# Optimization experiments

Hardware: AMD Instinct MI355X
Metric: run time of the kernel (lower is better)

Reference implementation:

```python
import math
import jax, jax.numpy as jnp
import numpy as np

B, H, T, N, D = 2, 4, 2048, 2048, 256
THETA = 2.0 ** 16


def setup_inputs() -> dict:
    key = jax.random.key(0)
    kq, kv = jax.random.split(key)
    Q = jax.random.normal(kq, (B, H, T, N), dtype=jnp.float32)
    V = jax.random.normal(kv, (B, 1, T, D), dtype=jnp.float32)
    return {"Q": Q, "V": V}


def _rope(Q):
    """BDH RoPE: freqs quantized in pairs, phases wrapped mod 1 then scaled to radians."""
    b, h, t, n = Q.shape
    # quantize(arange(n), 2) -> [0,0,2,2,4,4,...]
    idx = (jnp.arange(n) // 2 * 2).astype(jnp.float32)
    freqs = 1.0 / (THETA ** (idx / n)) / (2.0 * math.pi)            # (N,)
    pos = jnp.arange(t, dtype=jnp.float32)[:, None]                  # (T,1)
    phases = (pos * freqs) % 1.0 * (2.0 * math.pi)                   # (T,N)
    cos, sin = jnp.cos(phases), jnp.sin(phases)
    # rotate pairs: even slot <- -odd, odd slot <- even
    q2 = Q.reshape(b, h, t, n // 2, 2)
    Qrot = jnp.stack((-q2[..., 1], q2[..., 0]), axis=-1).reshape(b, h, t, n)
    return Q * cos + Qrot * sin


def reference(Q, V):
    QR = _rope(Q)                                                    # (B,H,T,N)
    scores = jnp.einsum('bhtn,bhsn->bhts', QR, QR)                   # (B,H,T,T), no softmax
    # strict lower-triangular causal mask (diagonal excluded), as in .tril(diagonal=-1)
    mask = jnp.tril(jnp.ones((scores.shape[-2], scores.shape[-1]), dtype=scores.dtype), k=-1)
    scores = scores * mask
    return jnp.matmul(scores, V)                                     # (B,H,T,D) via broadcast over H
```

## Files before the change

### kernel.cpp

```cpp
#include <hip/hip_runtime.h>
#include <stdint.h>

#define Tn 2048
#define Nn 2048
#define Dn 256
#define NHEAD 8
#define NKI 16

typedef __attribute__((ext_vector_type(8))) short short8;
typedef __attribute__((ext_vector_type(4))) float f32x4;
typedef __attribute__((ext_vector_type(4))) int i32x4;

__device__ __forceinline__ uint16_t f2bf(float x) {
  uint32_t u = __float_as_uint(x);
  return (uint16_t)((u + 0x7FFFu + ((u >> 16) & 1u)) >> 16);
}

__device__ __forceinline__ void gload_lds16(const void* g, void* l) {
  __builtin_amdgcn_global_load_lds((const __attribute__((address_space(1))) uint32_t*)g,
                                   (__attribute__((address_space(3))) uint32_t*)l,
                                   16, 0, 0);
}

__global__ __launch_bounds__(256) void rope_kernel(const float* __restrict__ Q,
                                                   uint8_t* __restrict__ QR,
                                                   float* __restrict__ Sc,
                                                   const float* __restrict__ V,
                                                   uint16_t* __restrict__ VT) {
  const int tid = threadIdx.x;
  const int bx = blockIdx.x;
  {
    int o = bx * 256 + tid;
    int vt = o & (Tn - 1);
    int vd = (o >> 11) & (Dn - 1);
    int vb = o >> 19;
    VT[o] = f2bf(V[((size_t)vb * Tn + vt) * Dn + vd]);
  }
  const int wv = tid >> 6, L = tid & 63;
  const int row = bx * 4 + wv;
  const int t = row & (Tn - 1);
  const float* src = Q + (size_t)row * Nn;

  float o[32];
  float am = 1e-8f;
#pragma unroll
  for (int k = 0; k < 8; ++k) {
    const float4 q = *(const float4*)(src + L * 4 + 256 * k);
    int p0 = 2 * L + 128 * k;
    float f0 = exp2f(-(float)p0 * (1.0f / 64.0f)) * 0.15915494309189535f;
    float f1 = exp2f(-(float)(p0 + 1) * (1.0f / 64.0f)) * 0.15915494309189535f;
    float x0 = (float)t * f0, x1 = (float)t * f1;
    float r0 = x0 - floorf(x0), r1 = x1 - floorf(x1);
    float s0 = __builtin_amdgcn_sinf(r0), c0 = __builtin_amdgcn_cosf(r0);
    float s1 = __builtin_amdgcn_sinf(r1), c1 = __builtin_amdgcn_cosf(r1);
    float o0 = q.x * c0 - q.y * s0;
    float o1 = q.y * c0 + q.x * s0;
    float o2 = q.z * c1 - q.w * s1;
    float o3 = q.w * c1 + q.z * s1;
    o[4 * k] = o0; o[4 * k + 1] = o1; o[4 * k + 2] = o2; o[4 * k + 3] = o3;
    am = fmaxf(am, fmaxf(fmaxf(fabsf(o0), fabsf(o1)), fmaxf(fabsf(o2), fabsf(o3))));
  }
#pragma unroll
  for (int off = 32; off > 0; off >>= 1) am = fmaxf(am, __shfl_xor(am, off));
  const float sc = 127.0f / am;
#pragma unroll
  for (int k = 0; k < 8; ++k) {
    int q0 = min(127, max(-127, (int)rintf(o[4 * k] * sc)));
    int q1 = min(127, max(-127, (int)rintf(o[4 * k + 1] * sc)));
    int q2 = min(127, max(-127, (int)rintf(o[4 * k + 2] * sc)));
    int q3 = min(127, max(-127, (int)rintf(o[4 * k + 3] * sc)));
    uint32_t pk = (uint32_t)(q0 & 255) | ((uint32_t)(q1 & 255) << 8) |
                  ((uint32_t)(q2 & 255) << 16) | ((uint32_t)q3 << 24);
    *(uint32_t*)(QR + (size_t)row * Nn + L * 4 + 256 * k) = pk;
  }
  if (L == 0) Sc[row] = am * (1.0f / 127.0f);
}

__global__ __launch_bounds__(256, 4) void qkt_kernel(const uint8_t* __restrict__ QR,
                                                     const float* __restrict__ Sc,
                                                     uint16_t* __restrict__ S) {
  __shared__ __align__(16) char lds0[32768];
  const int bx = blockIdx.x;
  const int g = bx & 7;
  int p = bx >> 3;
  int ti, tj; bool diag;
  if (p < 120) {
    ti = 1; while (p >= ti) { p -= ti; ++ti; }
    tj = p; diag = false;
  } else {
    ti = p - 120; tj = ti; diag = true;
  }

  const int tid = threadIdx.x;
  const int wv = tid >> 6, l = tid & 63, l15 = l & 15, lg = l >> 4;
  const int wi = wv >> 1;
  const int wj = wv & 1;
  const bool active = !(diag && wi == 0 && wj == 1);
  const bool needmask = diag && (wi == wj);

  const uint8_t* QRh = QR + (size_t)g * Tn * Nn;
  const int r0 = tid >> 3;
  const int scg = (tid & 7) ^ (r0 & 7);
  const uint8_t* gI = QRh + (size_t)(ti * 128 + r0) * Nn + scg * 16;
  const uint8_t* gJ = QRh + (size_t)(tj * 128 + r0) * Nn + scg * 16;

  char* bufI = lds0;
  char* bufJ = lds0 + 16384;

  i32x4 acc[4][4];
#pragma unroll
  for (int mi = 0; mi < 4; ++mi)
#pragma unroll
    for (int nj = 0; nj < 4; ++nj) acc[mi][nj] = (i32x4){0, 0, 0, 0};

  for (int k0 = 0; k0 < NKI; ++k0) {
    const int ke = k0 * 128;
    __syncthreads();
#pragma unroll
    for (int rnd = 0; rnd < 4; ++rnd) {
      gload_lds16(gI + (size_t)rnd * 32 * Nn + ke, bufI + rnd * 4096 + wv * 1024);
      if (!diag) gload_lds16(gJ + (size_t)rnd * 32 * Nn + ke, bufJ + rnd * 4096 + wv * 1024);
    }
    __syncthreads();
    if (active) {
      const char* bI = bufI;
      const char* bJ = diag ? bufI : bufJ;
#pragma unroll
      for (int ks = 0; ks < 2; ++ks) {
        i32x4 ifr[4], jfr[4];
#pragma unroll
        for (int mi = 0; mi < 4; ++mi) {
          int row = wi * 64 + mi * 16 + l15;
          int c = (ks * 4 + lg) ^ (row & 7);
          ifr[mi] = *(const i32x4*)(bI + row * 128 + c * 16);
        }
#pragma unroll
        for (int nj = 0; nj < 4; ++nj) {
          int row = wj * 64 + nj * 16 + l15;
          int c = (ks * 4 + lg) ^ (row & 7);
          jfr[nj] = *(const i32x4*)(bJ + row * 128 + c * 16);
        }
        __builtin_amdgcn_s_setprio(1);
#pragma unroll
        for (int mi = 0; mi < 4; ++mi)
#pragma unroll
          for (int nj = 0; nj < 4; ++nj)
            acc[mi][nj] = __builtin_amdgcn_mfma_i32_16x16x64_i8(jfr[nj], ifr[mi], acc[mi][nj], 0, 0, 0);
        __builtin_amdgcn_s_setprio(0);
      }
    }
  }

  uint16_t* Sh = S + (size_t)g * Tn * Tn;
  const float* ScI = Sc + g * Tn + ti * 128;
  const float* ScJ = Sc + g * Tn + tj * 128;
  if (active) {
#pragma unroll
    for (int mi = 0; mi < 4; ++mi) {
      int iloc = wi * 64 + mi * 16 + l15;
      float si = ScI[iloc];
#pragma unroll
      for (int nj = 0; nj < 4; ++nj) {
        int jloc = wj * 64 + nj * 16 + lg * 4;
        float4 sj = *(const float4*)(ScJ + jloc);
        i32x4 a = acc[mi][nj];
        float v0 = (float)a[0] * si * sj.x;
        float v1 = (float)a[1] * si * sj.y;
        float v2 = (float)a[2] * si * sj.z;
        float v3 = (float)a[3] * si * sj.w;
        if (needmask) {
          if (jloc + 0 >= iloc) v0 = 0.f;
          if (jloc + 1 >= iloc) v1 = 0.f;
          if (jloc + 2 >= iloc) v2 = 0.f;
          if (jloc + 3 >= iloc) v3 = 0.f;
        }
        uint32_t lo = (uint32_t)f2bf(v0) | ((uint32_t)f2bf(v1) << 16);
        uint32_t hi = (uint32_t)f2bf(v2) | ((uint32_t)f2bf(v3) << 16);
        *(uint2*)(Sh + (size_t)(ti * 128 + iloc) * Tn + tj * 128 + jloc) = make_uint2(lo, hi);
      }
    }
  } else {
#pragma unroll
    for (int mi = 0; mi < 4; ++mi)
#pragma unroll
      for (int nj = 0; nj < 4; ++nj) {
        int iloc = wi * 64 + mi * 16 + l15;
        int jloc = wj * 64 + nj * 16 + lg * 4;
        *(uint2*)(Sh + (size_t)(ti * 128 + iloc) * Tn + tj * 128 + jloc) = make_uint2(0u, 0u);
      }
  }
}

__global__ __launch_bounds__(512) void pv_kernel(const uint16_t* __restrict__ S,
                                                 const uint16_t* __restrict__ VT,
                                                 float* __restrict__ O) {
  extern __shared__ char lds[];
  const int bx = blockIdx.x;
  const int g = bx & 7;
  const int b = g >> 2;
  const int jid = bx >> 3;
  const int dh = jid & 1;
  const int ti = 31 - (jid >> 1);
  const int nsteps = ti + 1;

  const int tid = threadIdx.x;
  const int w = tid >> 6, l = tid & 63, l15 = l & 15, lg = l >> 4;
  const int ih = w >> 2;
  const int dq = w & 3;

  const uint16_t* Sh = S + (size_t)g * Tn * Tn;
  const uint16_t* VTb = VT + (size_t)b * Dn * Tn;
  const int r0 = tid >> 3;
  const int scg = (tid & 7) ^ (r0 & 7);
  const uint16_t* gS = Sh + (size_t)(ti * 64 + r0) * Tn + scg * 8;
  const uint16_t* gV = VTb + (size_t)(dh * 128 + r0) * Tn + scg * 8;

  f32x4 acc[2][2];
#pragma unroll
  for (int ma = 0; ma < 2; ++ma)
#pragma unroll
    for (int ni = 0; ni < 2; ++ni) acc[ma][ni] = (f32x4){0.f, 0.f, 0.f, 0.f};

  auto stage = [&](int ke, int bsel) {
    char* bufS = lds + bsel * 24576;
    char* bufV = bufS + 8192;
    gload_lds16(gS + ke, bufS + w * 1024);
    gload_lds16(gV + ke, bufV + w * 1024);
    gload_lds16(gV + (size_t)64 * Tn + ke, bufV + 8192 + w * 1024);
  };

  stage(0, 0);
  if (nsteps > 1) stage(64, 1);

  int cur = 0;
  for (int jt = 0; jt < nsteps; ++jt) {
    if (jt + 1 < nsteps) { asm volatile("s_waitcnt vmcnt(3)" ::: "memory"); }
    else                 { asm volatile("s_waitcnt vmcnt(0)" ::: "memory"); }
    __builtin_amdgcn_s_barrier();
    if (jt + 2 < nsteps) {
      int nb = cur + 2; if (nb >= 3) nb -= 3;
      stage((jt + 2) * 64, nb);
    }
    const char* bS = lds + cur * 24576;
    const char* bV = bS + 8192;
#pragma unroll
    for (int ks = 0; ks < 2; ++ks) {
      short8 av[2], bs[2];
#pragma unroll
      for (int ma = 0; ma < 2; ++ma) {
        int row = dq * 32 + ma * 16 + l15;
        int c = (ks * 4 + lg) ^ (row & 7);
        av[ma] = *(const short8*)(bV + row * 128 + c * 16);
      }
#pragma unroll
      for (int ni = 0; ni < 2; ++ni) {
        int row = ih * 32 + ni * 16 + l15;
        int c = (ks * 4 + lg) ^ (row & 7);
        bs[ni] = *(const short8*)(bS + row * 128 + c * 16);
      }
      __builtin_amdgcn_s_setprio(1);
#pragma unroll
      for (int ma = 0; ma < 2; ++ma)
#pragma unroll
        for (int ni = 0; ni < 2; ++ni)
          acc[ma][ni] = __builtin_amdgcn_mfma_f32_16x16x32_bf16(av[ma], bs[ni], acc[ma][ni], 0, 0, 0);
      __builtin_amdgcn_s_setprio(0);
    }
    ++cur; if (cur >= 3) cur = 0;
  }

  float* Oh = O + (size_t)g * Tn * Dn;
#pragma unroll
  for (int ma = 0; ma < 2; ++ma)
#pragma unroll
    for (int ni = 0; ni < 2; ++ni) {
      int iloc = ih * 32 + ni * 16 + l15;
      int d0 = dh * 128 + dq * 32 + ma * 16 + lg * 4;
      *(f32x4*)(Oh + (size_t)(ti * 64 + iloc) * Dn + d0) = acc[ma][ni];
    }
}

extern "C" void kernel_launch(void* const* d_in, const int* in_sizes, int n_in,
                              void* d_out, int out_size, void* d_ws, size_t ws_size,
                              hipStream_t stream) {
  const float* Q = (const float*)d_in[0];
  const float* V = (const float*)d_in[1];
  float* O = (float*)d_out;

  uint8_t* QRw = (uint8_t*)d_ws;
  float*   ScW = (float*)(QRw + (size_t)NHEAD * Tn * Nn);
  uint16_t* VTw = (uint16_t*)(ScW + (size_t)NHEAD * Tn);
  uint16_t* Sw  = VTw + (size_t)2 * Dn * Tn;

  hipFuncSetAttribute((const void*)pv_kernel, hipFuncAttributeMaxDynamicSharedMemorySize, 73728);

  rope_kernel<<<4096, 256, 0, stream>>>(Q, QRw, ScW, V, VTw);
  qkt_kernel<<<1088, 256, 0, stream>>>(QRw, ScW, Sw);
  pv_kernel<<<512, 512, 73728, stream>>>(Sw, VTw, O);
}
```

Measured before the change: 95.20 us.

## Use 128x64 QK^T tiles with finer triangular enumeration and higher occupancy

The QK^T kernel moves from 128x128 tiles, where diagonal tiles are handled specially, to 128x64 tiles. These are enumerated over the lower triangle at 64-column granularity, giving 272 tiles per head instead of 136. Masking now uses global indices, and launch bounds rise to 5 blocks per CU with less LDS per block. The intent is to cut wasted work above the diagonal and improve load balance and occupancy. The cost is lower arithmetic intensity per tile and more blocks that each reload the I rows.

```diff
diff --git a/kernel.cpp b/kernel.cpp
--- a/kernel.cpp
+++ b/kernel.cpp
@@ -6,6 +6,7 @@
 #define Dn 256
 #define NHEAD 8
 #define NKI 16
+#define JPH 272
 
 typedef __attribute__((ext_vector_type(8))) short short8;
 typedef __attribute__((ext_vector_type(4))) float f32x4;
@@ -76,75 +77,72 @@
   if (L == 0) Sc[row] = am * (1.0f / 127.0f);
 }
 
-__global__ __launch_bounds__(256, 4) void qkt_kernel(const uint8_t* __restrict__ QR,
+__global__ __launch_bounds__(256, 5) void qkt_kernel(const uint8_t* __restrict__ QR,
                                                      const float* __restrict__ Sc,
                                                      uint16_t* __restrict__ S) {
-  __shared__ __align__(16) char lds0[32768];
+  __shared__ __align__(16) char lds0[24576];
   const int bx = blockIdx.x;
   const int g = bx & 7;
   int p = bx >> 3;
-  int ti, tj; bool diag;
-  if (p < 120) {
-    ti = 1; while (p >= ti) { p -= ti; ++ti; }
-    tj = p; diag = false;
-  } else {
-    ti = p - 120; tj = ti; diag = true;
-  }
+  int ti = 0;
+  while (p >= 2 * ti + 2) { p -= 2 * ti + 2; ++ti; }
+  const int tj = p;
+  const bool needmask = (tj >= 2 * ti);
 
   const int tid = threadIdx.x;
   const int wv = tid >> 6, l = tid & 63, l15 = l & 15, lg = l >> 4;
   const int wi = wv >> 1;
   const int wj = wv & 1;
-  const bool active = !(diag && wi == 0 && wj == 1);
-  const bool needmask = diag && (wi == wj);
+  const int i0g = ti * 128 + wi * 64;
+  const int j0g = tj * 64 + wj * 32;
+  const bool active = !(needmask && j0g >= i0g + 63);
 
   const uint8_t* QRh = QR + (size_t)g * Tn * Nn;
   const int r0 = tid >> 3;
   const int scg = (tid & 7) ^ (r0 & 7);
   const uint8_t* gI = QRh + (size_t)(ti * 128 + r0) * Nn + scg * 16;
-  const uint8_t* gJ = QRh + (size_t)(tj * 128 + r0) * Nn + scg * 16;
+  const uint8_t* gJ = QRh + (size_t)(tj * 64 + r0) * Nn + scg * 16;
 
   char* bufI = lds0;
   char* bufJ = lds0 + 16384;
 
-  i32x4 acc[4][4];
+  i32x4 acc[4][2];
 #pragma unroll
   for (int mi = 0; mi < 4; ++mi)
 #pragma unroll
-    for (int nj = 0; nj < 4; ++nj) acc[mi][nj] = (i32x4){0, 0, 0, 0};
+    for (int nj = 0; nj < 2; ++nj) acc[mi][nj] = (i32x4){0, 0, 0, 0};
 
   for (int k0 = 0; k0 < NKI; ++k0) {
     const int ke = k0 * 128;
     __syncthreads();
 #pragma unroll
-    for (int rnd = 0; rnd < 4; ++rnd) {
+    for (int rnd = 0; rnd < 4; ++rnd)
       gload_lds16(gI + (size_t)rnd * 32 * Nn + ke, bufI + rnd * 4096 + wv * 1024);
-      if (!diag) gload_lds16(gJ + (size_t)rnd * 32 * Nn + ke, bufJ + rnd * 4096 + wv * 1024);
-    }
+#pragma unroll
+    for (int rnd = 0; rnd < 2; ++rnd)
+      gload_lds16(gJ + (size_t)rnd * 32 * Nn + ke, bufJ + rnd * 4096 + wv * 1024);
     __syncthreads();
     if (active) {
-      const char* bI = bufI;
-      const char* bJ = diag ? bufI : bufJ;
 #pragma unroll
       for (int ks = 0; ks < 2; ++ks) {
-        i32x4 ifr[4], jfr[4];
+        i32x4 ifr[4], jfr[2];
 #pragma unroll
         for (int mi = 0; mi < 4; ++mi) {
           int row = wi * 64 + mi * 16 + l15;
           int c = (ks * 4 + lg) ^ (row & 7);
-          ifr[mi] = *(const i32x4*)(bI + row * 128 + c * 16);
+          ifr[mi] = *(const i32x4*)(bufI + row * 128 + c * 16);
         }
 #pragma unroll
-        for (int nj = 0; nj < 4; ++nj) {
-          int row = wj * 64 + nj * 16 + l15;
+        for (int nj = 0; nj < 2; ++nj) {
+          int row = wj * 32 + nj * 16 + l15;
           int c = (ks * 4 + lg) ^ (row & 7);
-          jfr[nj] = *(const i32x4*)(bJ + row * 128 + c * 16);
+          jfr[nj] = *(const i32x4*)(bufJ + row * 128 + c * 16);
         }
         __builtin_amdgcn_s_setprio(1);
 #pragma unroll
         for (int mi = 0; mi < 4; ++mi)
 #pragma unroll
-          for (int nj = 0; nj < 4; ++nj)
+          for (int nj = 0; nj < 2; ++nj)
             acc[mi][nj] = __builtin_amdgcn_mfma_i32_16x16x64_i8(jfr[nj], ifr[mi], acc[mi][nj], 0, 0, 0);
         __builtin_amdgcn_s_setprio(0);
       }
@@ -153,41 +151,32 @@
 
   uint16_t* Sh = S + (size_t)g * Tn * Tn;
   const float* ScI = Sc + g * Tn + ti * 128;
-  const float* ScJ = Sc + g * Tn + tj * 128;
-  if (active) {
-#pragma unroll
-    for (int mi = 0; mi < 4; ++mi) {
-      int iloc = wi * 64 + mi * 16 + l15;
-      float si = ScI[iloc];
-#pragma unroll
-      for (int nj = 0; nj < 4; ++nj) {
-        int jloc = wj * 64 + nj * 16 + lg * 4;
-        float4 sj = *(const float4*)(ScJ + jloc);
-        i32x4 a = acc[mi][nj];
-        float v0 = (float)a[0] * si * sj.x;
-        float v1 = (float)a[1] * si * sj.y;
-        float v2 = (float)a[2] * si * sj.z;
-        float v3 = (float)a[3] * si * sj.w;
-        if (needmask) {
-          if (jloc + 0 >= iloc) v0 = 0.f;
-          if (jloc + 1 >= iloc) v1 = 0.f;
-          if (jloc + 2 >= iloc) v2 = 0.f;
-          if (jloc + 3 >= iloc) v3 = 0.f;
-        }
-        uint32_t lo = (uint32_t)f2bf(v0) | ((uint32_t)f2bf(v1) << 16);
-        uint32_t hi = (uint32_t)f2bf(v2) | ((uint32_t)f2bf(v3) << 16);
-        *(uint2*)(Sh + (size_t)(ti * 128 + iloc) * Tn + tj * 128 + jloc) = make_uint2(lo, hi);
-      }
-    }
-  } else {
-#pragma unroll
-    for (int mi = 0; mi < 4; ++mi)
-#pragma unroll
-      for (int nj = 0; nj < 4; ++nj) {
-        int iloc = wi * 64 + mi * 16 + l15;
-        int jloc = wj * 64 + nj * 16 + lg * 4;
-        *(uint2*)(Sh + (size_t)(ti * 128 + iloc) * Tn + tj * 128 + jloc) = make_uint2(0u, 0u);
-      }
+  const float* ScJ = Sc + g * Tn + tj * 64;
+#pragma unroll
+  for (int mi = 0; mi < 4; ++mi) {
+    int iloc = wi * 64 + mi * 16 + l15;
+    float si = ScI[iloc];
+    int ig = ti * 128 + iloc;
+#pragma unroll
+    for (int nj = 0; nj < 2; ++nj) {
+      int jloc = wj * 32 + nj * 16 + lg * 4;
+      int jg = tj * 64 + jloc;
+      float4 sj = *(const float4*)(ScJ + jloc);
+      i32x4 a = acc[mi][nj];
+      float v0 = (float)a[0] * si * sj.x;
+      float v1 = (float)a[1] * si * sj.y;
+      float v2 = (float)a[2] * si * sj.z;
+      float v3 = (float)a[3] * si * sj.w;
+      if (needmask) {
+        if (jg + 0 >= ig) v0 = 0.f;
+        if (jg + 1 >= ig) v1 = 0.f;
+        if (jg + 2 >= ig) v2 = 0.f;
+        if (jg + 3 >= ig) v3 = 0.f;
+      }
+      uint32_t lo = (uint32_t)f2bf(v0) | ((uint32_t)f2bf(v1) << 16);
+      uint32_t hi = (uint32_t)f2bf(v2) | ((uint32_t)f2bf(v3) << 16);
+      *(uint2*)(Sh + (size_t)ig * Tn + jg) = make_uint2(lo, hi);
+    }
   }
 }
 
@@ -295,6 +284,6 @@
   hipFuncSetAttribute((const void*)pv_kernel, hipFuncAttributeMaxDynamicSharedMemorySize, 73728);
 
   rope_kernel<<<4096, 256, 0, stream>>>(Q, QRw, ScW, V, VTw);
-  qkt_kernel<<<1088, 256, 0, stream>>>(QRw, ScW, Sw);
+  qkt_kernel<<<NHEAD * JPH, 256, 0, stream>>>(QRw, ScW, Sw);
   pv_kernel<<<512, 512, 73728, stream>>>(Sw, VTw, O);
 }
```

After: 97.88 us. 1.03x slower.
